# Kernel tuning notes

Hardware: AMD Instinct MI355X
Metric: run time of the kernel (lower is better)

The kernel has to match this reference:

```python
import jax, jax.numpy as jnp
import numpy as np

B, S, D = 2, 2048, 2048
QH, KVH, HD = 32, 8, 64
GRP = QH // KVH  # GQA group size = 4


def setup_inputs() -> dict:
    key = jax.random.key(0)
    ks = jax.random.split(key, 9)
    x = jax.random.normal(ks[0], (B, S, D), jnp.float32)
    # RoPE angle table: [S, HD//2] -> stacked (cos, sin) -> [S, HD//2, 2]
    inv_freq = 1.0 / (10000.0 ** (np.arange(0, HD, 2, dtype=np.float32) / HD))
    ang = np.arange(S, dtype=np.float32)[:, None] * inv_freq[None, :]
    freqs = jnp.stack([jnp.cos(jnp.asarray(ang)), jnp.sin(jnp.asarray(ang))], axis=-1).astype(jnp.float32)
    w = 0.02
    Wq = jax.random.normal(ks[1], (D, QH * HD), jnp.float32) * w
    bq = jnp.zeros((QH * HD,), jnp.float32)
    Wk = jax.random.normal(ks[2], (D, KVH * HD), jnp.float32) * w
    bk = jnp.zeros((KVH * HD,), jnp.float32)
    Wv = jax.random.normal(ks[3], (D, KVH * HD), jnp.float32) * w
    bv = jnp.zeros((KVH * HD,), jnp.float32)
    Wo = jax.random.normal(ks[4], (QH * HD, D), jnp.float32) * w
    bo = jnp.zeros((D,), jnp.float32)
    return {"x": x, "freqs": freqs, "Wq": Wq, "bq": bq, "Wk": Wk, "bk": bk,
            "Wv": Wv, "bv": bv, "Wo": Wo, "bo": bo}


def _rope(xh, cos, sin):
    # xh: [b, s, h, hd]; complex rotation on adjacent pairs, like view_as_complex
    b, s, h, hd = xh.shape
    xp = xh.reshape(b, s, h, hd // 2, 2)
    x0, x1 = xp[..., 0], xp[..., 1]
    o0 = x0 * cos - x1 * sin
    o1 = x0 * sin + x1 * cos
    return jnp.stack([o0, o1], axis=-1).reshape(b, s, h, hd)


def reference(x, freqs, Wq, bq, Wk, bk, Wv, bv, Wo, bo):
    b, s, _ = x.shape
    q = (x @ Wq + bq).reshape(b, s, QH, HD)
    k = (x @ Wk + bk).reshape(b, s, KVH, HD)
    v = (x @ Wv + bv).reshape(b, s, KVH, HD)
    cos = freqs[:s, :, 0][None, :, None, :]  # [1, s, 1, hd//2]
    sin = freqs[:s, :, 1][None, :, None, :]
    q = _rope(q, cos, sin)
    k = _rope(k, cos, sin)
    # [b, h, s, hd]
    q = q.transpose(0, 2, 1, 3).reshape(b, KVH, GRP, s, HD)
    k = k.transpose(0, 2, 1, 3)  # [b, kvh, s, hd]
    v = v.transpose(0, 2, 1, 3)
    scores = jnp.einsum('bkgsh,bkth->bkgst', q, k) / jnp.sqrt(jnp.float32(HD))
    attn = jax.nn.softmax(scores, axis=-1)
    o = jnp.einsum('bkgst,bkth->bkgsh', attn, v)  # [b, kvh, grp, s, hd]
    o = o.reshape(b, QH, s, HD).transpose(0, 2, 1, 3).reshape(b, s, QH * HD)
    return o @ Wo + bo
```

## Files before the change

kernel.cpp:

```cpp
#include <hip/hip_runtime.h>
#include <stdint.h>

#define B_   2
#define S_   2048
#define D_   2048
#define QH_  32
#define KVH_ 8
#define HD_  64

typedef short  short8  __attribute__((ext_vector_type(8)));
typedef float  floatx4 __attribute__((ext_vector_type(4)));

__device__ __forceinline__ ushort f2b(float f) {
  union { float f; uint32_t u; } c; c.f = f;
  uint32_t u = c.u;
  return (ushort)((u + 0x7FFFu + ((u >> 16) & 1u)) >> 16);
}

__device__ __forceinline__ uint32_t fbits(float f) {
  union { float f; uint32_t u; } c; c.f = f;
  return c.u;
}

__device__ __forceinline__ short8 mk8(uint32_t a, uint32_t b, uint32_t c, uint32_t d) {
  union { uint4 u; short8 s; } v; v.u = (uint4){a, b, c, d}; return v.s;
}

__device__ __forceinline__ uint32_t cvtpk(float a, float b) {
  uint32_t r;
  asm("v_cvt_pk_bf16_f32 %0, %1, %2" : "=v"(r) : "v"(a), "v"(b));
  return r;
}

__device__ __forceinline__ void dma16(const void* g, void* l) {
  __builtin_amdgcn_global_load_lds(
      (const __attribute__((address_space(1))) uint32_t*)(uintptr_t)g,
      (__attribute__((address_space(3))) uint32_t*)(uintptr_t)l, 16, 0, 0);
}

#define QSCALE 0.18033688f


__global__ __launch_bounds__(256) void conv_x_kernel(const float* __restrict__ X,
                                                     ushort* __restrict__ Xb) {
  size_t i = ((size_t)blockIdx.x * 256 + threadIdx.x) * 4;
  float4 v = *(const float4*)(X + i);
  ushort4 o;
  o.x = f2b(v.x); o.y = f2b(v.y); o.z = f2b(v.z); o.w = f2b(v.w);
  *(ushort4*)(Xb + i) = o;
}

__global__ void tconv_all_kernel(const float* __restrict__ Wq, const float* __restrict__ Wk,
                                 const float* __restrict__ Wv, const float* __restrict__ Wo,
                                 ushort* __restrict__ wqkv, ushort* __restrict__ wo) {
  __shared__ float tile[32][33];
  int z = blockIdx.z;
  const float* W; ushort* Wt; int N;
  if (z == 0)      { W = Wq; Wt = wqkv;                        N = 2048; }
  else if (z == 1) { W = Wk; Wt = wqkv + (size_t)2048 * 2048;  N = 512;  }
  else if (z == 2) { W = Wv; Wt = wqkv + (size_t)2560 * 2048;  N = 512;  }
  else             { W = Wo; Wt = wo;                          N = 2048; }
  int bx = blockIdx.x, by = blockIdx.y;
  if (bx * 32 >= N) return;
  int tx = threadIdx.x, ty = threadIdx.y;
#pragma unroll
  for (int i = 0; i < 32; i += 8)
    tile[ty + i][tx] = W[(size_t)(by * 32 + ty + i) * N + bx * 32 + tx];
  __syncthreads();
#pragma unroll
  for (int i = 0; i < 32; i += 8)
    Wt[(size_t)(bx * 32 + ty + i) * 2048 + by * 32 + tx] = f2b(tile[tx][ty + i]);
}


__global__ __launch_bounds__(256) void gemm_qkv_kernel(
    const ushort* __restrict__ A, const ushort* __restrict__ Bt,
    const float* __restrict__ bq, const float* __restrict__ bk,
    const float* __restrict__ bv, const float2* __restrict__ F2,
    ushort* __restrict__ qb, ushort* __restrict__ kb, ushort* __restrict__ vt) {
  const int K = 2048;
  __shared__ ushort sA[2][128 * 32];
  __shared__ ushort sB[2][128 * 32];
  const int tid  = threadIdx.x;
  const int bm   = blockIdx.y, bn = blockIdx.x;
  const int wave = tid >> 6, lane = tid & 63;
  const int quad = lane >> 4, l16 = lane & 15;
  const int wm   = (wave >> 1) * 64, wn = (wave & 1) * 64;

  const ushort* Ab = A  + (size_t)(bm * 128) * K;
  const ushort* Bb = Bt + (size_t)(bn * 128) * K;

  const int gr = lane >> 2;
  const int gu = (lane & 3) * 8;

  floatx4 acc[4][4];
#pragma unroll
  for (int i = 0; i < 4; i++)
#pragma unroll
    for (int j = 0; j < 4; j++) acc[i][j] = (floatx4){0.f, 0.f, 0.f, 0.f};

#pragma unroll
  for (int j = 0; j < 2; j++) {
    int row = j * 64 + wave * 16 + gr;
    dma16(Ab + (size_t)row * K + gu, &sA[0][j * 2048 + wave * 512]);
    dma16(Bb + (size_t)row * K + gu, &sB[0][j * 2048 + wave * 512]);
  }

  int cur = 0;
  for (int k0 = 0; k0 < K; k0 += 32) {
    __syncthreads();
    if (k0 + 32 < K) {
      int nxt = cur ^ 1;
#pragma unroll
      for (int j = 0; j < 2; j++) {
        int row = j * 64 + wave * 16 + gr;
        dma16(Ab + (size_t)row * K + k0 + 32 + gu, &sA[nxt][j * 2048 + wave * 512]);
        dma16(Bb + (size_t)row * K + k0 + 32 + gu, &sB[nxt][j * 2048 + wave * 512]);
      }
    }
    short8 af[4], bf[4];
#pragma unroll
    for (int mi = 0; mi < 4; mi++)
      af[mi] = *(const short8*)&sA[cur][(wm + mi * 16 + l16) * 32 + quad * 8];
#pragma unroll
    for (int ni = 0; ni < 4; ni++)
      bf[ni] = *(const short8*)&sB[cur][(wn + ni * 16 + l16) * 32 + quad * 8];
#pragma unroll
    for (int mi = 0; mi < 4; mi++)
#pragma unroll
      for (int ni = 0; ni < 4; ni++)
        acc[mi][ni] = __builtin_amdgcn_mfma_f32_16x16x32_bf16(
            af[mi], bf[ni], acc[mi][ni], 0, 0, 0);
    cur ^= 1;
  }

  const int isQ = (bn < 16);
  const int isV = (bn >= 20);
  const int hh  = wn >> 6;
  const float sySign = (l16 & 1) ? 1.f : -1.f;

  const float* bsrc = isQ ? bq : (isV ? bv : bk);
  const int    boff = isQ ? 0  : (isV ? 2560 : 2048);

  float bvv[4];
#pragma unroll
  for (int ni = 0; ni < 4; ni++)
    bvv[ni] = bsrc[bn * 128 + wn + ni * 16 + l16 - boff];

  if (!isV) {
    ushort* dst = isQ ? qb : kb;
    const int NH    = isQ ? QH_ : KVH_;
    const int hbase = isQ ? (bn * 2 + hh) : ((bn - 16) * 2 + hh);
#pragma unroll
    for (int mi = 0; mi < 4; mi++) {
#pragma unroll
      for (int r = 0; r < 4; r++) {
        int row = bm * 128 + wm + mi * 16 + quad * 4 + r;
        int s = row & 2047, bb = row >> 11;
        size_t base = (((size_t)bb * NH + hbase) * S_ + s) * HD_ + l16 * 4;
        float o[4];
#pragma unroll
        for (int ni = 0; ni < 4; ni++) {
          float xv = acc[mi][ni][r] + bvv[ni];
          float2 cs = F2[s * 32 + ni * 8 + (l16 >> 1)];
          float pp = __shfl_xor(xv, 1);
          float oo = fmaf(pp * sySign, cs.y, xv * cs.x);
          if (isQ) oo *= QSCALE;
          o[ni] = oo;
        }
        ushort4 pk;
        pk.x = f2b(o[0]); pk.y = f2b(o[1]); pk.z = f2b(o[2]); pk.w = f2b(o[3]);
        *(ushort4*)&dst[base] = pk;
      }
    }
  } else {
    const int h = (bn - 20) * 2 + hh;
#pragma unroll
    for (int mi = 0; mi < 4; mi++) {
      int row0 = bm * 128 + wm + mi * 16 + quad * 4;
      int bb   = row0 >> 11;
      int posb = ((row0 & 2047) & ~63) + (mi & 2) * 16 + quad * 8 + (mi & 1) * 4;
#pragma unroll
      for (int ni = 0; ni < 4; ni++) {
        int dt = ni * 16 + l16;
        ushort4 st;
        st.x = f2b(acc[mi][ni][0] + bvv[ni]);
        st.y = f2b(acc[mi][ni][1] + bvv[ni]);
        st.z = f2b(acc[mi][ni][2] + bvv[ni]);
        st.w = f2b(acc[mi][ni][3] + bvv[ni]);
        *(ushort4*)&vt[(((size_t)bb * 8 + h) * 64 + dt) * (size_t)S_ + posb] = st;
      }
    }
  }
}


__global__ __launch_bounds__(256) void gemm_bt_kernel(
    const ushort* __restrict__ A, const ushort* __restrict__ Bt,
    const float* __restrict__ bias, float* __restrict__ C,
    int M, int N, int K) {
  __shared__ ushort sA[2][128 * 32];
  __shared__ ushort sB[2][128 * 32];
  const int tid  = threadIdx.x;
  const int bm   = blockIdx.y, bn = blockIdx.x;
  const int wave = tid >> 6, lane = tid & 63;
  const int quad = lane >> 4, l16 = lane & 15;
  const int wm   = (wave >> 1) * 64, wn = (wave & 1) * 64;

  const ushort* Ab = A  + (size_t)(bm * 128) * K;
  const ushort* Bb = Bt + (size_t)(bn * 128) * K;

  const int gr = lane >> 2;
  const int gu = (lane & 3) * 8;

  floatx4 acc[4][4];
#pragma unroll
  for (int i = 0; i < 4; i++)
#pragma unroll
    for (int j = 0; j < 4; j++) acc[i][j] = (floatx4){0.f, 0.f, 0.f, 0.f};

#pragma unroll
  for (int j = 0; j < 2; j++) {
    int row = j * 64 + wave * 16 + gr;
    dma16(Ab + (size_t)row * K + gu, &sA[0][j * 2048 + wave * 512]);
    dma16(Bb + (size_t)row * K + gu, &sB[0][j * 2048 + wave * 512]);
  }

  int cur = 0;
  for (int k0 = 0; k0 < K; k0 += 32) {
    __syncthreads();
    if (k0 + 32 < K) {
      int nxt = cur ^ 1;
#pragma unroll
      for (int j = 0; j < 2; j++) {
        int row = j * 64 + wave * 16 + gr;
        dma16(Ab + (size_t)row * K + k0 + 32 + gu, &sA[nxt][j * 2048 + wave * 512]);
        dma16(Bb + (size_t)row * K + k0 + 32 + gu, &sB[nxt][j * 2048 + wave * 512]);
      }
    }
    short8 af[4], bf[4];
#pragma unroll
    for (int mi = 0; mi < 4; mi++)
      af[mi] = *(const short8*)&sA[cur][(wm + mi * 16 + l16) * 32 + quad * 8];
#pragma unroll
    for (int ni = 0; ni < 4; ni++)
      bf[ni] = *(const short8*)&sB[cur][(wn + ni * 16 + l16) * 32 + quad * 8];
#pragma unroll
    for (int mi = 0; mi < 4; mi++)
#pragma unroll
      for (int ni = 0; ni < 4; ni++)
        acc[mi][ni] = __builtin_amdgcn_mfma_f32_16x16x32_bf16(
            af[mi], bf[ni], acc[mi][ni], 0, 0, 0);
    cur ^= 1;
  }

#pragma unroll
  for (int mi = 0; mi < 4; mi++) {
#pragma unroll
    for (int ni = 0; ni < 4; ni++) {
      int col  = bn * 128 + wn + ni * 16 + l16;
      float bv = bias[col];
#pragma unroll
      for (int r = 0; r < 4; r++) {
        int row = bm * 128 + wm + mi * 16 + quad * 4 + r;
        C[(size_t)row * N + col] = acc[mi][ni][r] + bv;
      }
    }
  }
}


__global__ __launch_bounds__(512, 4) void attn_kernel(
    const ushort* __restrict__ Q, const ushort* __restrict__ K,
    const ushort* __restrict__ Vt, ushort* __restrict__ O) {
  const int id  = blockIdx.x + 8 * (blockIdx.y + 32 * blockIdx.z);
  const int kvh = id & 7;
  const int qt  = (id >> 3) & 7;
  const int qh  = kvh * 4 + ((id >> 6) & 3);
  const int b   = id >> 8;
  const int tid = threadIdx.x;
  const int wave = tid >> 6, lane = tid & 63;
  const int quad = lane >> 4, l16 = lane & 15;

  __shared__ ushort kBuf[2][64 * 64];
  __shared__ ushort vBuf[2][64 * 64];

  const ushort* Qh = Q  + ((size_t)(b * QH_ + qh)) * S_ * HD_;
  const ushort* Kh = K  + ((size_t)(b * KVH_ + kvh)) * S_ * HD_;
  const ushort* Vh = Vt + ((size_t)(b * KVH_ + kvh)) * HD_ * S_;

  const int dr = lane >> 3;
  const int du = (lane & 7) ^ (dr & 7);
  const size_t kLaneOff = (size_t)(wave * 8 + dr) * 64 + du * 8;
  const size_t vLaneOff = (size_t)(wave * 8 + dr) * S_ + du * 8;
  const int swz = l16 & 7;

  const int q0 = qt * 256 + wave * 32;
  short8 aq[2][2];
#pragma unroll
  for (int m = 0; m < 2; m++)
#pragma unroll
    for (int s2 = 0; s2 < 2; s2++)
      aq[m][s2] = *(const short8*)(Qh + (size_t)(q0 + m * 16 + l16) * HD_ + s2 * 32 + quad * 8);

  floatx4 oacc[2][4];
#pragma unroll
  for (int m = 0; m < 2; m++)
#pragma unroll
    for (int t = 0; t < 4; t++) oacc[m][t] = (floatx4){0.f, 0.f, 0.f, 0.f};
  float ls[2] = {0.f, 0.f};

  dma16(Kh + kLaneOff, &kBuf[0][wave * 512]);
  dma16(Vh + vLaneOff, &vBuf[0][wave * 512]);

  int cur = 0;
  for (int kv0 = 0; kv0 < S_; kv0 += 64) {
    __syncthreads();
    if (kv0 + 64 < S_) {
      int nxt = cur ^ 1;
      dma16(Kh + (size_t)(kv0 + 64) * 64 + kLaneOff, &kBuf[nxt][wave * 512]);
      dma16(Vh + (size_t)(kv0 + 64) + vLaneOff,      &vBuf[nxt][wave * 512]);
    }

    floatx4 sc[2][2][2];
    __builtin_amdgcn_s_setprio(1);
#pragma unroll
    for (int u = 0; u < 2; u++) {
#pragma unroll
      for (int cc = 0; cc < 2; cc++) {
        const int c = u * 2 + cc;
        short8 kf0 = *(const short8*)&kBuf[cur][(c * 16 + l16) * 64 + ((quad ^ swz) * 8)];
        short8 kf1 = *(const short8*)&kBuf[cur][(c * 16 + l16) * 64 + (((4 + quad) ^ swz) * 8)];
#pragma unroll
        for (int m = 0; m < 2; m++) {
          floatx4 s0 = (floatx4){0.f, 0.f, 0.f, 0.f};
          s0 = __builtin_amdgcn_mfma_f32_16x16x32_bf16(kf0, aq[m][0], s0, 0, 0, 0);
          sc[u][cc][m] = __builtin_amdgcn_mfma_f32_16x16x32_bf16(kf1, aq[m][1], s0, 0, 0, 0);
        }
      }
    }
    __builtin_amdgcn_s_setprio(0);

    uint32_t pk[2][2][4];
#pragma unroll
    for (int u = 0; u < 2; u++)
#pragma unroll
      for (int cc = 0; cc < 2; cc++)
#pragma unroll
        for (int m = 0; m < 2; m++) {
          float p0 = __builtin_amdgcn_exp2f(sc[u][cc][m][0]);
          float p1 = __builtin_amdgcn_exp2f(sc[u][cc][m][1]);
          float p2 = __builtin_amdgcn_exp2f(sc[u][cc][m][2]);
          float p3 = __builtin_amdgcn_exp2f(sc[u][cc][m][3]);
          ls[m] += (p0 + p1) + (p2 + p3);
          pk[u][m][cc * 2 + 0] = cvtpk(p0, p1);
          pk[u][m][cc * 2 + 1] = cvtpk(p2, p3);
        }

#pragma unroll
    for (int u = 0; u < 2; u++) {
      short8 ap[2];
#pragma unroll
      for (int m = 0; m < 2; m++)
        ap[m] = mk8(pk[u][m][0], pk[u][m][1], pk[u][m][2], pk[u][m][3]);
      __builtin_amdgcn_s_setprio(1);
#pragma unroll
      for (int t = 0; t < 4; t++) {
        const int row = (t * 16 + l16) * 64;
        short8 vf = *(const short8*)&vBuf[cur][row + (((u * 4 + quad) ^ swz) * 8)];
#pragma unroll
        for (int m = 0; m < 2; m++)
          oacc[m][t] = __builtin_amdgcn_mfma_f32_16x16x32_bf16(ap[m], vf, oacc[m][t], 0, 0, 0);
      }
      __builtin_amdgcn_s_setprio(0);
    }
    cur ^= 1;
  }

#pragma unroll
  for (int m = 0; m < 2; m++) {
    ls[m] += __shfl_xor(ls[m], 16);
    ls[m] += __shfl_xor(ls[m], 32);
  }
#pragma unroll
  for (int m = 0; m < 2; m++) {
#pragma unroll
    for (int r = 0; r < 4; r++) {
      float l = __shfl(ls[m], (lane & 48) | (quad * 4 + r));
      float inv = 1.0f / l;
      int srow = q0 + m * 16 + quad * 4 + r;
      size_t base = ((size_t)b * S_ + srow) * (QH_ * HD_) + (size_t)qh * HD_;
#pragma unroll
      for (int t = 0; t < 4; t++)
        O[base + t * 16 + l16] = f2b(oacc[m][t][r] * inv);
    }
  }
}


extern "C" void kernel_launch(void* const* d_in, const int* in_sizes, int n_in,
                              void* d_out, int out_size, void* d_ws, size_t ws_size,
                              hipStream_t stream) {
  const float* x  = (const float*)d_in[0];
  const float* fr = (const float*)d_in[1];
  const float* Wq = (const float*)d_in[2];
  const float* bq = (const float*)d_in[3];
  const float* Wk = (const float*)d_in[4];
  const float* bk = (const float*)d_in[5];
  const float* Wv = (const float*)d_in[6];
  const float* bv = (const float*)d_in[7];
  const float* Wo = (const float*)d_in[8];
  const float* bo = (const float*)d_in[9];
  float* out = (float*)d_out;
  char* ws = (char*)d_ws;

  ushort* xb    = (ushort*)(ws + 0);
  ushort* wqkv  = (ushort*)(ws + 16777216);
  ushort* wo    = (ushort*)(ws + 29360128);
  ushort* qb    = (ushort*)(ws + 37761024);
  ushort* kb    = (ushort*)(ws + 54538240);
  ushort* vt    = (ushort*)(ws + 62926848);
  ushort* ob    = xb;

  conv_x_kernel<<<8192, 256, 0, stream>>>(x, xb);
  tconv_all_kernel<<<dim3(64, 64, 4), dim3(32, 8), 0, stream>>>(Wq, Wk, Wv, Wo, wqkv, wo);

  gemm_qkv_kernel<<<dim3(3072 / 128, 4096 / 128), 256, 0, stream>>>(
      xb, wqkv, bq, bk, bv, (const float2*)fr, qb, kb, vt);

  attn_kernel<<<dim3(8, 32, 2), 512, 0, stream>>>(qb, kb, vt, ob);

  gemm_bt_kernel<<<dim3(2048 / 128, 4096 / 128), 256, 0, stream>>>(
      ob, wo, bo, out, 4096, 2048, 2048);
}
```

Baseline: 323.3 us.

## Enlarge attention KV tile to 128, interleave softmax with MFMA, swizzle GEMM blocks

The attention kernel now streams K/V in 128-row tiles instead of 64, which halves the number of barriers and DMA rounds, and it fuses the exp/pack step into each 32-column chunk so PV MFMAs follow directly. The output GEMM remaps block ids so neighbouring workgroups share rows of A and B, aiming at better L2 reuse. The QKV GEMM gains an occupancy hint in its launch bounds. In exchange the attention kernel uses twice the LDS, which may lower occupancy under its 512-thread, 4-block bound.

```diff
diff --git a/kernel.cpp b/kernel.cpp
--- a/kernel.cpp
+++ b/kernel.cpp
@@ -73,7 +73,7 @@
 }
 
 
-__global__ __launch_bounds__(256) void gemm_qkv_kernel(
+__global__ __launch_bounds__(256, 5) void gemm_qkv_kernel(
     const ushort* __restrict__ A, const ushort* __restrict__ Bt,
     const float* __restrict__ bq, const float* __restrict__ bk,
     const float* __restrict__ bv, const float2* __restrict__ F2,
@@ -202,7 +202,9 @@
   __shared__ ushort sA[2][128 * 32];
   __shared__ ushort sB[2][128 * 32];
   const int tid  = threadIdx.x;
-  const int bm   = blockIdx.y, bn = blockIdx.x;
+  const int wg   = blockIdx.y * gridDim.x + blockIdx.x;
+  const int id   = (wg & 7) * 64 + (wg >> 3);
+  const int bm   = id >> 4, bn = id & 15;
   const int wave = tid >> 6, lane = tid & 63;
   const int quad = lane >> 4, l16 = lane & 15;
   const int wm   = (wave >> 1) * 64, wn = (wave & 1) * 64;
@@ -282,17 +284,21 @@
   const int wave = tid >> 6, lane = tid & 63;
   const int quad = lane >> 4, l16 = lane & 15;
 
-  __shared__ ushort kBuf[2][64 * 64];
-  __shared__ ushort vBuf[2][64 * 64];
+  __shared__ ushort kBuf[2][128 * 64];
+  __shared__ ushort vBuf[2][64 * 128];
 
   const ushort* Qh = Q  + ((size_t)(b * QH_ + qh)) * S_ * HD_;
   const ushort* Kh = K  + ((size_t)(b * KVH_ + kvh)) * S_ * HD_;
   const ushort* Vh = Vt + ((size_t)(b * KVH_ + kvh)) * HD_ * S_;
 
-  const int dr = lane >> 3;
-  const int du = (lane & 7) ^ (dr & 7);
-  const size_t kLaneOff = (size_t)(wave * 8 + dr) * 64 + du * 8;
-  const size_t vLaneOff = (size_t)(wave * 8 + dr) * S_ + du * 8;
+  const int dr  = lane >> 3;
+  const int du  = (lane & 7) ^ (dr & 7);
+  const size_t kOff0 = (size_t)(wave * 16 + 0 + dr) * 64 + du * 8;
+  const size_t kOff1 = (size_t)(wave * 16 + 8 + dr) * 64 + du * 8;
+  const int vd0 = wave * 8 + 0 + (lane >> 4);
+  const int vd1 = wave * 8 + 4 + (lane >> 4);
+  const size_t vOff0 = (size_t)vd0 * S_ + (size_t)((((lane & 15) ^ (vd0 & 7))) * 8);
+  const size_t vOff1 = (size_t)vd1 * S_ + (size_t)((((lane & 15) ^ (vd1 & 7))) * 8);
   const int swz = l16 & 7;
 
   const int q0 = qt * 256 + wave * 32;
@@ -310,22 +316,25 @@
     for (int t = 0; t < 4; t++) oacc[m][t] = (floatx4){0.f, 0.f, 0.f, 0.f};
   float ls[2] = {0.f, 0.f};
 
-  dma16(Kh + kLaneOff, &kBuf[0][wave * 512]);
-  dma16(Vh + vLaneOff, &vBuf[0][wave * 512]);
+  dma16(Kh + kOff0, &kBuf[0][wave * 1024]);
+  dma16(Kh + kOff1, &kBuf[0][wave * 1024 + 512]);
+  dma16(Vh + vOff0, &vBuf[0][wave * 1024]);
+  dma16(Vh + vOff1, &vBuf[0][wave * 1024 + 512]);
 
   int cur = 0;
-  for (int kv0 = 0; kv0 < S_; kv0 += 64) {
+  for (int kv0 = 0; kv0 < S_; kv0 += 128) {
     __syncthreads();
-    if (kv0 + 64 < S_) {
+    if (kv0 + 128 < S_) {
       int nxt = cur ^ 1;
-      dma16(Kh + (size_t)(kv0 + 64) * 64 + kLaneOff, &kBuf[nxt][wave * 512]);
-      dma16(Vh + (size_t)(kv0 + 64) + vLaneOff,      &vBuf[nxt][wave * 512]);
-    }
-
-    floatx4 sc[2][2][2];
-    __builtin_amdgcn_s_setprio(1);
-#pragma unroll
-    for (int u = 0; u < 2; u++) {
+      dma16(Kh + (size_t)(kv0 + 128) * 64 + kOff0, &kBuf[nxt][wave * 1024]);
+      dma16(Kh + (size_t)(kv0 + 128) * 64 + kOff1, &kBuf[nxt][wave * 1024 + 512]);
+      dma16(Vh + (size_t)(kv0 + 128) + vOff0,      &vBuf[nxt][wave * 1024]);
+      dma16(Vh + (size_t)(kv0 + 128) + vOff1,      &vBuf[nxt][wave * 1024 + 512]);
+    }
+
+#pragma unroll
+    for (int u = 0; u < 4; u++) {
+      uint32_t pk[2][4];
 #pragma unroll
       for (int cc = 0; cc < 2; cc++) {
         const int c = u * 2 + cc;
@@ -333,46 +342,32 @@
         short8 kf1 = *(const short8*)&kBuf[cur][(c * 16 + l16) * 64 + (((4 + quad) ^ swz) * 8)];
 #pragma unroll
         for (int m = 0; m < 2; m++) {
-          floatx4 s0 = (floatx4){0.f, 0.f, 0.f, 0.f};
-          s0 = __builtin_amdgcn_mfma_f32_16x16x32_bf16(kf0, aq[m][0], s0, 0, 0, 0);
-          sc[u][cc][m] = __builtin_amdgcn_mfma_f32_16x16x32_bf16(kf1, aq[m][1], s0, 0, 0, 0);
+          floatx4 sc = (floatx4){0.f, 0.f, 0.f, 0.f};
+          __builtin_amdgcn_s_setprio(1);
+          sc = __builtin_amdgcn_mfma_f32_16x16x32_bf16(kf0, aq[m][0], sc, 0, 0, 0);
+          sc = __builtin_amdgcn_mfma_f32_16x16x32_bf16(kf1, aq[m][1], sc, 0, 0, 0);
+          __builtin_amdgcn_s_setprio(0);
+          float p0 = __builtin_amdgcn_exp2f(sc[0]);
+          float p1 = __builtin_amdgcn_exp2f(sc[1]);
+          float p2 = __builtin_amdgcn_exp2f(sc[2]);
+          float p3 = __builtin_amdgcn_exp2f(sc[3]);
+          ls[m] += (p0 + p1) + (p2 + p3);
+          pk[m][cc * 2 + 0] = cvtpk(p0, p1);
+          pk[m][cc * 2 + 1] = cvtpk(p2, p3);
         }
       }
-    }
-    __builtin_amdgcn_s_setprio(0);
-
-    uint32_t pk[2][2][4];
-#pragma unroll
-    for (int u = 0; u < 2; u++)
-#pragma unroll
-      for (int cc = 0; cc < 2; cc++)
+#pragma unroll
+      for (int t = 0; t < 4; t++) {
+        const int row = (t * 16 + l16) * 128;
+        short8 vf = *(const short8*)&vBuf[cur][row + (((u * 4 + quad) ^ swz) * 8)];
+        __builtin_amdgcn_s_setprio(1);
 #pragma unroll
         for (int m = 0; m < 2; m++) {
-          float p0 = __builtin_amdgcn_exp2f(sc[u][cc][m][0]);
-          float p1 = __builtin_amdgcn_exp2f(sc[u][cc][m][1]);
-          float p2 = __builtin_amdgcn_exp2f(sc[u][cc][m][2]);
-          float p3 = __builtin_amdgcn_exp2f(sc[u][cc][m][3]);
-          ls[m] += (p0 + p1) + (p2 + p3);
-          pk[u][m][cc * 2 + 0] = cvtpk(p0, p1);
-          pk[u][m][cc * 2 + 1] = cvtpk(p2, p3);
+          short8 ap = mk8(pk[m][0], pk[m][1], pk[m][2], pk[m][3]);
+          oacc[m][t] = __builtin_amdgcn_mfma_f32_16x16x32_bf16(ap, vf, oacc[m][t], 0, 0, 0);
         }
-
-#pragma unroll
-    for (int u = 0; u < 2; u++) {
-      short8 ap[2];
-#pragma unroll
-      for (int m = 0; m < 2; m++)
-        ap[m] = mk8(pk[u][m][0], pk[u][m][1], pk[u][m][2], pk[u][m][3]);
-      __builtin_amdgcn_s_setprio(1);
-#pragma unroll
-      for (int t = 0; t < 4; t++) {
-        const int row = (t * 16 + l16) * 64;
-        short8 vf = *(const short8*)&vBuf[cur][row + (((u * 4 + quad) ^ swz) * 8)];
-#pragma unroll
-        for (int m = 0; m < 2; m++)
-          oacc[m][t] = __builtin_amdgcn_mfma_f32_16x16x32_bf16(ap[m], vf, oacc[m][t], 0, 0, 0);
-      }
-      __builtin_amdgcn_s_setprio(0);
+        __builtin_amdgcn_s_setprio(0);
+      }
     }
     cur ^= 1;
   }
```

Measured after the change: 348.5 us. +7.8%, slower.
